# Optimization experiments

Hardware: AMD Instinct MI355X
Metric: run time of the kernel (lower is better)

The kernel has to match this reference:

```python
import jax, jax.numpy as jnp
import numpy as np
from jax import lax


def setup_inputs() -> dict:
    key = jax.random.key(0)
    ks = jax.random.split(key, 16)
    f32 = jnp.float32
    g = lambda k, shp, s=0.02: jax.random.normal(k, shp, dtype=f32) * s
    inp = {
        "x": jax.random.normal(ks[0], (4, 1, 4096), dtype=f32),
        # conv_time: Conv1d(1,128,3,pad=1)
        "conv_time_w": g(ks[1], (128, 1, 3)), "conv_time_b": jnp.zeros((128,), f32),
        "bn0_g": jnp.ones((128,), f32), "bn0_b": jnp.zeros((128,), f32),
        "bn0_m": jnp.zeros((128,), f32), "bn0_v": jnp.ones((128,), f32),
        # block1: Conv1d(128,256,3,pad=1)+BN
        "conv1_w": g(ks[2], (256, 128, 3)), "conv1_b": jnp.zeros((256,), f32),
        "bn1_g": jnp.ones((256,), f32), "bn1_b": jnp.zeros((256,), f32),
        "bn1_m": jnp.zeros((256,), f32), "bn1_v": jnp.ones((256,), f32),
        # block2: Conv1d(256,512,3,pad=1)+BN
        "conv2_w": g(ks[3], (512, 256, 3)), "conv2_b": jnp.zeros((512,), f32),
        "bn2_g": jnp.ones((512,), f32), "bn2_b": jnp.zeros((512,), f32),
        "bn2_m": jnp.zeros((512,), f32), "bn2_v": jnp.ones((512,), f32),
        # GAT 1: fc Linear(512,512), attn_fc Linear(1024,1)
        "gat1_fc_w": g(ks[4], (512, 512)), "gat1_fc_b": jnp.zeros((512,), f32),
        "gat1_attn_w": g(ks[5], (1024,)), "gat1_attn_b": jnp.zeros((), f32),
        # GAT 2: fc Linear(512,256), attn_fc Linear(512,1)
        "gat2_fc_w": g(ks[6], (256, 512)), "gat2_fc_b": jnp.zeros((256,), f32),
        "gat2_attn_w": g(ks[7], (512,)), "gat2_attn_b": jnp.zeros((), f32),
        # head: Linear(256,2)
        "fc_w": g(ks[8], (2, 256)), "fc_b": jnp.zeros((2,), f32),
    }
    return inp


def _conv1d(x, w, b):
    # x: [B,C,T], w: [O,C,3], padding=1
    y = lax.conv_general_dilated(x, w, window_strides=(1,), padding=((1, 1),),
                                 dimension_numbers=("NCH", "OIH", "NCH"))
    return y + b[None, :, None]


def _bn(x, g, b, m, v):
    # eval-mode BatchNorm1d over channel dim
    return (x - m[None, :, None]) * (g * lax.rsqrt(v + 1e-5))[None, :, None] + b[None, :, None]


def _maxpool2(x):
    return lax.reduce_window(x, -jnp.inf, lax.max, (1, 1, 2), (1, 1, 2), "VALID")


def _gat(x2d, fc_w, fc_b, aw, ab):
    # Faithful to: cat([h_i, h_j]) @ attn_w == h_i @ aw[:d] + h_j @ aw[d:]
    h = x2d @ fc_w.T + fc_b           # [N, d]
    d = h.shape[-1]
    s1 = h @ aw[:d]                   # [N] (query part, h.repeat(1,N))
    s2 = h @ aw[d:]                   # [N] (key part,   h.repeat(N,1))
    e = jax.nn.leaky_relu(s1[:, None] + s2[None, :] + ab, negative_slope=0.01)  # [N,N]
    att = jax.nn.softmax(e, axis=1)
    return att @ h                    # [N, d]


def reference(x, conv_time_w, conv_time_b, bn0_g, bn0_b, bn0_m, bn0_v,
              conv1_w, conv1_b, bn1_g, bn1_b, bn1_m, bn1_v,
              conv2_w, conv2_b, bn2_g, bn2_b, bn2_m, bn2_v,
              gat1_fc_w, gat1_fc_b, gat1_attn_w, gat1_attn_b,
              gat2_fc_w, gat2_fc_b, gat2_attn_w, gat2_attn_b,
              fc_w, fc_b):
    h = jax.nn.relu(_bn(_conv1d(x, conv_time_w, conv_time_b), bn0_g, bn0_b, bn0_m, bn0_v))
    h = _maxpool2(jax.nn.relu(_bn(_conv1d(h, conv1_w, conv1_b), bn1_g, bn1_b, bn1_m, bn1_v)))
    h = _maxpool2(jax.nn.relu(_bn(_conv1d(h, conv2_w, conv2_b), bn2_g, bn2_b, bn2_m, bn2_v)))
    h = jnp.transpose(h, (0, 2, 1))   # [B, S, 512]
    B, S, C = h.shape
    g = h.reshape(B * S, C)           # whole batch flattened into one graph (as in source)
    g = _gat(g, gat1_fc_w, gat1_fc_b, gat1_attn_w, gat1_attn_b)   # [N, 512]
    g = _gat(g, gat2_fc_w, gat2_fc_b, gat2_attn_w, gat2_attn_b)   # [N, 256]
    pooled = g.reshape(B, S, -1).mean(axis=1)                     # [B, 256]
    return pooled @ fc_w.T + fc_b     # [B, 2] (dropout is identity in eval)
```

## Files before the change

### kernel.cpp

```cpp
#include <hip/hip_runtime.h>
#include <hip/hip_bf16.h>
#include <math.h>


#define NN 4096
#define BB 4

__global__ void k_conv_time3(const float* __restrict__ x, const float* __restrict__ w,
                             const float* __restrict__ cb, const float* __restrict__ g,
                             const float* __restrict__ bbp, const float* __restrict__ m,
                             const float* __restrict__ v, float* __restrict__ out) {
  int gid = blockIdx.x * 256 + threadIdx.x;
  int t4 = gid & 1023;
  int o = (gid >> 10) & 127;
  int b = gid >> 17;
  int t = t4 * 4;
  float sc = g[o] * rsqrtf(v[o] + 1e-5f);
  float sh = (cb[o] - m[o]) * sc + bbp[o];
  const float* xb = x + b * 4096;
  float4 xc = *(const float4*)&xb[t];
  float xm = (t > 0) ? xb[t - 1] : 0.f;
  float xp = (t + 4 < 4096) ? xb[t + 4] : 0.f;
  const float* wo = w + o * 3;
  float w0 = wo[0], w1 = wo[1], w2 = wo[2];
  float4 y;
  y.x = fmaxf((w0 * xm   + w1 * xc.x + w2 * xc.y) * sc + sh, 0.f);
  y.y = fmaxf((w0 * xc.x + w1 * xc.y + w2 * xc.z) * sc + sh, 0.f);
  y.z = fmaxf((w0 * xc.y + w1 * xc.z + w2 * xc.w) * sc + sh, 0.f);
  y.w = fmaxf((w0 * xc.z + w1 * xc.w + w2 * xp  ) * sc + sh, 0.f);
  float* orow = out + ((size_t)(b * 128) + o) * 4104 + 4;
  *(float4*)&orow[t] = y;
  if (t4 == 0)    { orow[-4] = 0.f; orow[-3] = 0.f; orow[-2] = 0.f; orow[-1] = 0.f; }
  if (t4 == 1023) { orow[4096] = 0.f; orow[4097] = 0.f; orow[4098] = 0.f; orow[4099] = 0.f; }
}

template <int C, int TIN, int OPAD>
__global__ __launch_bounds__(256, 8)
void k_conv_quad(const float* __restrict__ in, const float* __restrict__ w,
                 const float* __restrict__ cb, const float* __restrict__ g,
                 const float* __restrict__ bbp, const float* __restrict__ m,
                 const float* __restrict__ v, float* __restrict__ out, int OCH) {
  constexpr int TOUT = TIN / 2;
  constexpr int IST = TIN + 8;
  constexpr int QC = C / 4;
  const int OST = TOUT + 2 * OPAD;
  __shared__ float red[3][16][64];

  int nT = TIN / 256;
  int bx = blockIdx.x;
  int tb = bx % nT;
  int oq = (bx / nT) % (OCH / 4);
  int b  = bx / (nT * (OCH / 4));
  int tid = threadIdx.x;
  int lane = tid & 63;
  int wv = __builtin_amdgcn_readfirstlane(tid >> 6);
  int t0 = tb * 256;

  float acc[4][4];
  #pragma unroll
  for (int oi = 0; oi < 4; oi++)
    #pragma unroll
    for (int p = 0; p < 4; p++) acc[oi][p] = 0.f;

  const float* wq = w + (size_t)(oq * 4) * C * 3 + (size_t)(wv * QC) * 3;
  const float* xb = in + ((size_t)(b * C) + wv * QC) * IST + 4 + t0 + 4 * lane;

  float4 A = *(const float4*)(xb - 1);
  float2 Bv = *(const float2*)(xb + 3);
  for (int cc = 0; cc < QC; ++cc) {
    float4 An; float2 Bn;
    if (cc + 1 < QC) {
      const float* nx = xb + (size_t)(cc + 1) * IST;
      An = *(const float4*)(nx - 1);
      Bn = *(const float2*)(nx + 3);
    }
    const float* wr = wq + (size_t)cc * 3;
    #pragma unroll
    for (int oi = 0; oi < 4; oi++) {
      const float* wo = wr + (size_t)oi * C * 3;
      float w0 = wo[0], w1 = wo[1], w2 = wo[2];
      acc[oi][0] += w0 * A.x + w1 * A.y + w2 * A.z;
      acc[oi][1] += w0 * A.y + w1 * A.z + w2 * A.w;
      acc[oi][2] += w0 * A.z + w1 * A.w + w2 * Bv.x;
      acc[oi][3] += w0 * A.w + w1 * Bv.x + w2 * Bv.y;
    }
    A = An; Bv = Bn;
  }

  if (wv != 0) {
    #pragma unroll
    for (int oi = 0; oi < 4; oi++)
      #pragma unroll
      for (int p = 0; p < 4; p++)
        red[wv - 1][oi * 4 + p][lane] = acc[oi][p];
  }
  __syncthreads();
  if (wv == 0) {
    int base_o = oq * 4;
    #pragma unroll
    for (int oi = 0; oi < 4; oi++) {
      int o = base_o + oi;
      float sc = g[o] * rsqrtf(v[o] + 1e-5f);
      float sh = (cb[o] - m[o]) * sc + bbp[o];
      float y0 = acc[oi][0] + red[0][oi * 4 + 0][lane] + red[1][oi * 4 + 0][lane] + red[2][oi * 4 + 0][lane];
      float y1 = acc[oi][1] + red[0][oi * 4 + 1][lane] + red[1][oi * 4 + 1][lane] + red[2][oi * 4 + 1][lane];
      float y2 = acc[oi][2] + red[0][oi * 4 + 2][lane] + red[1][oi * 4 + 2][lane] + red[2][oi * 4 + 2][lane];
      float y3 = acc[oi][3] + red[0][oi * 4 + 3][lane] + red[1][oi * 4 + 3][lane] + red[2][oi * 4 + 3][lane];
      float2 r;
      r.x = fmaxf(fmaxf(y0 * sc + sh, y1 * sc + sh), 0.f);
      r.y = fmaxf(fmaxf(y2 * sc + sh, y3 * sc + sh), 0.f);
      *(float2*)&out[((size_t)(b * OCH) + o) * OST + OPAD + tb * 128 + 2 * lane] = r;
    }
    if (OPAD > 0 && tb == 0) {
      if (lane < 4) {
        float* row = out + ((size_t)(b * OCH) + base_o + lane) * OST;
        row[0] = 0.f; row[1] = 0.f; row[2] = 0.f; row[3] = 0.f;
      } else if (lane < 8) {
        float* row = out + ((size_t)(b * OCH) + base_o + lane - 4) * OST;
        row[OPAD + TOUT + 0] = 0.f; row[OPAD + TOUT + 1] = 0.f;
        row[OPAD + TOUT + 2] = 0.f; row[OPAD + TOUT + 3] = 0.f;
      }
    }
  }
}

__global__ __launch_bounds__(512, 4)
void k_gemm_chw(const float* __restrict__ A, const float* __restrict__ Wt,
                const float* __restrict__ bias, float* __restrict__ Cout) {
  constexpr int K = 512, N = 512;
  __shared__ float As[32][132];
  __shared__ float Bs[32][68];
  int i0 = blockIdx.x * 128, j0 = blockIdx.y * 64;
  int tid = threadIdx.x;
  int tx = tid & 15, ty = tid >> 4;
  int b = i0 >> 10, s0 = i0 & 1023;
  const float* Ab = A + (size_t)b * K * 1024 + s0;

  float acc[4][4];
  #pragma unroll
  for (int ii = 0; ii < 4; ii++)
    #pragma unroll
    for (int jj = 0; jj < 4; jj++) acc[ii][jj] = 0.f;

  int ka = (tid + 0) >> 5, i4a = tid & 31;
  int kb = (tid + 512) >> 5, i4b = tid & 31;
  float4 pa0, pa1; float pb[4];

  pa0 = *(const float4*)&Ab[(size_t)ka * 1024 + 4 * i4a];
  pa1 = *(const float4*)&Ab[(size_t)kb * 1024 + 4 * i4b];
  #pragma unroll
  for (int r = 0; r < 4; r++) {
    int e = tid + 512 * r; int j = e >> 5, k = e & 31;
    pb[r] = Wt[(size_t)(j0 + j) * K + k];
  }

  for (int kt = 0; kt < K; kt += 32) {
    *(float4*)&As[ka][4 * i4a] = pa0;
    *(float4*)&As[kb][4 * i4b] = pa1;
    #pragma unroll
    for (int r = 0; r < 4; r++) {
      int e = tid + 512 * r; int j = e >> 5, k = e & 31;
      Bs[k][j] = pb[r];
    }
    __syncthreads();
    int ktn = (kt + 32 < K) ? kt + 32 : 0;
    float4 na0 = *(const float4*)&Ab[(size_t)(ktn + ka) * 1024 + 4 * i4a];
    float4 na1 = *(const float4*)&Ab[(size_t)(ktn + kb) * 1024 + 4 * i4b];
    float nb[4];
    #pragma unroll
    for (int r = 0; r < 4; r++) {
      int e = tid + 512 * r; int j = e >> 5, k = e & 31;
      nb[r] = Wt[(size_t)(j0 + j) * K + ktn + k];
    }
    #pragma unroll 4
    for (int kk = 0; kk < 32; ++kk) {
      float4 a4 = *(const float4*)&As[kk][ty * 4];
      float4 b4 = *(const float4*)&Bs[kk][tx * 4];
      float a[4] = {a4.x, a4.y, a4.z, a4.w};
      float bv[4] = {b4.x, b4.y, b4.z, b4.w};
      #pragma unroll
      for (int ii = 0; ii < 4; ii++)
        #pragma unroll
        for (int jj = 0; jj < 4; jj++) acc[ii][jj] += a[ii] * bv[jj];
    }
    __syncthreads();
    pa0 = na0; pa1 = na1;
    #pragma unroll
    for (int r = 0; r < 4; r++) pb[r] = nb[r];
  }

  float4 bias4 = *(const float4*)&bias[j0 + 4 * tx];
  #pragma unroll
  for (int ii = 0; ii < 4; ii++) {
    int i = i0 + ty * 4 + ii;
    float4 o4;
    o4.x = acc[ii][0] + bias4.x; o4.y = acc[ii][1] + bias4.y;
    o4.z = acc[ii][2] + bias4.z; o4.w = acc[ii][3] + bias4.w;
    *(float4*)&Cout[(size_t)i * N + j0 + 4 * tx] = o4;
  }
}

__global__ __launch_bounds__(256, 4)
void k_gemm_rm(const float* __restrict__ A, const float* __restrict__ Wt,
               const float* __restrict__ bias, float* __restrict__ Cout) {
  constexpr int K = 512, N = 256;
  __shared__ float As[32][68];
  __shared__ float Bs[32][68];
  int i0 = blockIdx.x * 64, j0 = blockIdx.y * 64;
  int tid = threadIdx.x;
  int tx = tid & 15, ty = tid >> 4;

  float acc[4][4];
  #pragma unroll
  for (int ii = 0; ii < 4; ii++)
    #pragma unroll
    for (int jj = 0; jj < 4; jj++) acc[ii][jj] = 0.f;

  float4 pa[2]; float pb[8];
  #pragma unroll
  for (int r = 0; r < 2; r++) {
    int e4 = tid + 256 * r; int i = e4 >> 3, k4 = e4 & 7;
    pa[r] = *(const float4*)&A[(size_t)(i0 + i) * K + 4 * k4];
  }
  #pragma unroll
  for (int r = 0; r < 8; r++) {
    int e = tid + 256 * r; int j = e >> 5, k = e & 31;
    pb[r] = Wt[(size_t)(j0 + j) * K + k];
  }

  for (int kt = 0; kt < K; kt += 32) {
    #pragma unroll
    for (int r = 0; r < 2; r++) {
      int e4 = tid + 256 * r; int i = e4 >> 3, k4 = e4 & 7;
      As[4 * k4 + 0][i] = pa[r].x; As[4 * k4 + 1][i] = pa[r].y;
      As[4 * k4 + 2][i] = pa[r].z; As[4 * k4 + 3][i] = pa[r].w;
    }
    #pragma unroll
    for (int r = 0; r < 8; r++) {
      int e = tid + 256 * r; int j = e >> 5, k = e & 31;
      Bs[k][j] = pb[r];
    }
    __syncthreads();
    int ktn = (kt + 32 < K) ? kt + 32 : 0;
    float4 na[2]; float nb[8];
    #pragma unroll
    for (int r = 0; r < 2; r++) {
      int e4 = tid + 256 * r; int i = e4 >> 3, k4 = e4 & 7;
      na[r] = *(const float4*)&A[(size_t)(i0 + i) * K + ktn + 4 * k4];
    }
    #pragma unroll
    for (int r = 0; r < 8; r++) {
      int e = tid + 256 * r; int j = e >> 5, k = e & 31;
      nb[r] = Wt[(size_t)(j0 + j) * K + ktn + k];
    }
    #pragma unroll 4
    for (int kk = 0; kk < 32; ++kk) {
      float4 a4 = *(const float4*)&As[kk][ty * 4];
      float4 b4 = *(const float4*)&Bs[kk][tx * 4];
      float a[4] = {a4.x, a4.y, a4.z, a4.w};
      float bv[4] = {b4.x, b4.y, b4.z, b4.w};
      #pragma unroll
      for (int ii = 0; ii < 4; ii++)
        #pragma unroll
        for (int jj = 0; jj < 4; jj++) acc[ii][jj] += a[ii] * bv[jj];
    }
    __syncthreads();
    pa[0] = na[0]; pa[1] = na[1];
    #pragma unroll
    for (int r = 0; r < 8; r++) pb[r] = nb[r];
  }

  float4 bias4 = *(const float4*)&bias[j0 + 4 * tx];
  #pragma unroll
  for (int ii = 0; ii < 4; ii++) {
    int i = i0 + ty * 4 + ii;
    float4 o4;
    o4.x = acc[ii][0] + bias4.x; o4.y = acc[ii][1] + bias4.y;
    o4.z = acc[ii][2] + bias4.z; o4.w = acc[ii][3] + bias4.w;
    *(float4*)&Cout[(size_t)i * N + j0 + 4 * tx] = o4;
  }
}

template <int D>
__global__ void k_rowdot(const float* __restrict__ h, const float* __restrict__ aw,
                         float* __restrict__ s1, float* __restrict__ s2,
                         int* __restrict__ rnk) {
  if (blockIdx.x < 16) rnk[blockIdx.x * 256 + threadIdx.x] = 0;
  int wid = threadIdx.x >> 6, lane = threadIdx.x & 63;
  int i = blockIdx.x * 4 + wid;
  const float* hr = h + (size_t)i * D;
  float d1 = 0.f, d2 = 0.f;
  #pragma unroll
  for (int d = lane; d < D; d += 64) {
    float hv = hr[d];
    d1 += hv * aw[d];
    d2 += hv * aw[D + d];
  }
  for (int off = 32; off; off >>= 1) {
    d1 += __shfl_down(d1, off, 64);
    d2 += __shfl_down(d2, off, 64);
  }
  if (lane == 0) { s1[i] = d1; s2[i] = d2; }
}

__global__ void k_rank(const float* __restrict__ s2v, int* __restrict__ rnk) {
  __shared__ float ls[1024];
  int j = blockIdx.x * 256 + threadIdx.x;
  int base = blockIdx.y * 1024;
  float vj = s2v[j];
  for (int e = threadIdx.x; e < 1024; e += 256) ls[e] = s2v[base + e];
  __syncthreads();
  int cnt = 0;
  #pragma unroll 8
  for (int r = 0; r < 1024; ++r) {
    float vr = ls[r];
    cnt += (vr < vj || (vr == vj && (base + r) < j)) ? 1 : 0;
  }
  atomicAdd(&rnk[j], cnt);
}

__global__ void k_scatter(const float* __restrict__ s2v, const int* __restrict__ rnk,
                          float* __restrict__ svals, int* __restrict__ sidx) {
  int j = blockIdx.x * 256 + threadIdx.x;
  int r = rnk[j];
  svals[r] = s2v[j];
  sidx[r] = j;
}

__global__ void k_scan_den(const float* __restrict__ svals,
                           float* __restrict__ preden, float* __restrict__ sufden) {
  __shared__ float csP[256], csM[256];
  int tid = threadIdx.x;
  int base = tid * 16;
  float M2 = svals[NN - 1];
  float lwp[16], lwm[16];
  #pragma unroll
  for (int u = 0; u < 16; u++) {
    float d = svals[base + u] - M2;
    lwp[u] = expf(d);
    lwm[u] = expf(0.01f * d);
  }
  float sm = 0.f, sp = 0.f;
  #pragma unroll
  for (int u = 0; u < 16; u++) { sm += lwm[u]; sp += lwp[u]; }
  csM[tid] = sm; csP[tid] = sp;
  __syncthreads();
  float offM = 0.f;
  for (int c = 0; c < tid; c++) offM += csM[c];
  float offP = 0.f;
  for (int c = tid + 1; c < 256; c++) offP += csP[c];
  float run = offM;
  #pragma unroll
  for (int u = 0; u < 16; u++) { preden[base + u] = run; run += lwm[u]; }
  if (tid == 255) preden[NN] = run;
  float runp = offP;
  if (tid == 255) sufden[NN] = 0.f;
  #pragma unroll
  for (int u = 15; u >= 0; u--) { runp += lwp[u]; sufden[base + u] = runp; }
}

template <int D>
__global__ void k_chunksum(const float* __restrict__ h, const int* __restrict__ sidx,
                           const float* __restrict__ svals,
                           float* __restrict__ csP, float* __restrict__ csM) {
  constexpr int CPT = D / 256;
  int c = blockIdx.x, tid = threadIdx.x;
  __shared__ int lidx[32];
  __shared__ float lwp[32], lwm[32];
  if (tid < 32) {
    int r = c * 32 + tid;
    float d = svals[r] - svals[NN - 1];
    lidx[tid] = sidx[r]; lwp[tid] = expf(d); lwm[tid] = expf(0.01f * d);
  }
  __syncthreads();
  float aP[CPT], aM[CPT];
  #pragma unroll
  for (int q = 0; q < CPT; q++) { aP[q] = 0.f; aM[q] = 0.f; }
  for (int u = 0; u < 32; u++) {
    const float* hr = h + (size_t)lidx[u] * D;
    float fp = lwp[u], fm = lwm[u];
    #pragma unroll
    for (int q = 0; q < CPT; q++) {
      float hv = hr[tid + q * 256];
      aP[q] += fp * hv; aM[q] += fm * hv;
    }
  }
  #pragma unroll
  for (int q = 0; q < CPT; q++) {
    csP[(size_t)c * D + tid + q * 256] = aP[q];
    csM[(size_t)c * D + tid + q * 256] = aM[q];
  }
}

template <int D>
__global__ void k_chunkoff(const float* __restrict__ csP, const float* __restrict__ csM,
                           float* __restrict__ offP, float* __restrict__ offM) {
  int d = blockIdx.x * 128 + threadIdx.x;
  float rm = 0.f;
  for (int cb = 0; cb < 128; cb += 16) {
    float vals[16];
    #pragma unroll
    for (int u = 0; u < 16; u++) vals[u] = csM[(size_t)(cb + u) * D + d];
    #pragma unroll
    for (int u = 0; u < 16; u++) { offM[(size_t)(cb + u) * D + d] = rm; rm += vals[u]; }
  }
  float rp = 0.f;
  for (int cb = 127; cb >= 15; cb -= 16) {
    float vals[16];
    #pragma unroll
    for (int u = 0; u < 16; u++) vals[u] = csP[(size_t)(cb - u) * D + d];
    #pragma unroll
    for (int u = 0; u < 16; u++) { offP[(size_t)(cb - u) * D + d] = rp; rp += vals[u]; }
  }
}

template <int D>
__global__ void k_scanwrite(const float* __restrict__ h, const int* __restrict__ sidx,
                            const float* __restrict__ svals,
                            const float* __restrict__ offP, const float* __restrict__ offM,
                            float* __restrict__ Pre, float* __restrict__ Suf) {
  constexpr int CPT = D / 256;
  int c = blockIdx.x, tid = threadIdx.x;
  __shared__ int lidx[32];
  __shared__ float lwp[32], lwm[32];
  if (tid < 32) {
    int r = c * 32 + tid;
    float d = svals[r] - svals[NN - 1];
    lidx[tid] = sidx[r]; lwp[tid] = expf(d); lwm[tid] = expf(0.01f * d);
  }
  __syncthreads();
  float runM[CPT], runP[CPT];
  #pragma unroll
  for (int q = 0; q < CPT; q++) {
    int d = tid + q * 256;
    runM[q] = offM[(size_t)c * D + d];
    runP[q] = offP[(size_t)c * D + d];
  }
  for (int u = 0; u < 32; u++) {
    const float* hr = h + (size_t)lidx[u] * D;
    float fm = lwm[u];
    #pragma unroll
    for (int q = 0; q < CPT; q++) {
      int d = tid + q * 256;
      Pre[(size_t)(c * 32 + u) * D + d] = runM[q];
      runM[q] += fm * hr[d];
    }
  }
  if (c == 127) {
    #pragma unroll
    for (int q = 0; q < CPT; q++) Pre[(size_t)NN * D + tid + q * 256] = runM[q];
    #pragma unroll
    for (int q = 0; q < CPT; q++) Suf[(size_t)NN * D + tid + q * 256] = 0.f;
  }
  for (int u = 31; u >= 0; u--) {
    const float* hr = h + (size_t)lidx[u] * D;
    float fp = lwp[u];
    #pragma unroll
    for (int q = 0; q < CPT; q++) {
      int d = tid + q * 256;
      runP[q] += fp * hr[d];
      Suf[(size_t)(c * 32 + u) * D + d] = runP[q];
    }
  }
}

template <int D>
__global__ void k_apply(const float* __restrict__ Pre, const float* __restrict__ Suf,
                        const float* __restrict__ preden, const float* __restrict__ sufden,
                        const float* __restrict__ s1, const float* __restrict__ svals,
                        const float* __restrict__ abp, float* __restrict__ outg) {
  int i = blockIdx.x;
  float ab = abp[0], M2 = svals[NN - 1];
  float alpha = s1[i] + ab;
  float cthr = -alpha;
  int lo = 0, hi = NN;
  while (lo < hi) {
    int mid = (lo + hi) >> 1;
    if (svals[mid] < cthr) lo = mid + 1; else hi = mid;
  }
  int t = lo;
  float e1 = alpha + M2;
  float gam = fmaxf(e1, 0.01f * e1);
  float A = expf(e1 - gam);
  float Bv = expf(0.01f * e1 - gam);
  float den = A * sufden[t] + Bv * preden[t];
  float inv = 1.f / den;
  const float* Pr = Pre + (size_t)t * D;
  const float* Sr = Suf + (size_t)t * D;
  for (int d = threadIdx.x; d < D; d += 256)
    outg[(size_t)i * D + d] = (A * Sr[d] + Bv * Pr[d]) * inv;
}

__global__ void k_pool(const float* __restrict__ g2, float* __restrict__ pp) {
  int b = blockIdx.x >> 4, ch = blockIdx.x & 15;
  const float* base = g2 + ((size_t)(b * 1024) + ch * 64) * 256 + threadIdx.x;
  float s = 0.f;
  for (int r = 0; r < 64; r++) s += base[(size_t)r * 256];
  pp[(size_t)blockIdx.x * 256 + threadIdx.x] = s;
}

__global__ void k_head2(const float* __restrict__ pp, const float* __restrict__ fcw,
                        const float* __restrict__ fcb, float* __restrict__ out) {
  __shared__ float pooled[4][256];
  int tid = threadIdx.x;
  for (int b = 0; b < 4; b++) {
    float s = 0.f;
    for (int ch = 0; ch < 16; ch++) s += pp[(size_t)(b * 16 + ch) * 256 + tid];
    pooled[b][tid] = s * (1.f / 1024.f);
  }
  __syncthreads();
  if (tid < 8) {
    int b = tid >> 1, c = tid & 1;
    float acc = fcb[c];
    for (int cc = 0; cc < 256; cc++) acc += pooled[b][cc] * fcw[c * 256 + cc];
    out[b * 2 + c] = acc;
  }
}

extern "C" void kernel_launch(void* const* d_in, const int* in_sizes, int n_in,
                              void* d_out, int out_size, void* d_ws, size_t ws_size,
                              hipStream_t stream) {
  const float* x    = (const float*)d_in[0];
  const float* ctw  = (const float*)d_in[1];
  const float* ctb  = (const float*)d_in[2];
  const float* bn0g = (const float*)d_in[3];
  const float* bn0b = (const float*)d_in[4];
  const float* bn0m = (const float*)d_in[5];
  const float* bn0v = (const float*)d_in[6];
  const float* c1w  = (const float*)d_in[7];
  const float* c1b  = (const float*)d_in[8];
  const float* bn1g = (const float*)d_in[9];
  const float* bn1b = (const float*)d_in[10];
  const float* bn1m = (const float*)d_in[11];
  const float* bn1v = (const float*)d_in[12];
  const float* c2w  = (const float*)d_in[13];
  const float* c2b  = (const float*)d_in[14];
  const float* bn2g = (const float*)d_in[15];
  const float* bn2b = (const float*)d_in[16];
  const float* bn2m = (const float*)d_in[17];
  const float* bn2v = (const float*)d_in[18];
  const float* g1w  = (const float*)d_in[19];
  const float* g1b  = (const float*)d_in[20];
  const float* g1aw = (const float*)d_in[21];
  const float* g1ab = (const float*)d_in[22];
  const float* g2w  = (const float*)d_in[23];
  const float* g2b  = (const float*)d_in[24];
  const float* g2aw = (const float*)d_in[25];
  const float* g2ab = (const float*)d_in[26];
  const float* fcw  = (const float*)d_in[27];
  const float* fcb  = (const float*)d_in[28];
  float* ws = (float*)d_ws;

  const size_t S0SZ = (size_t)4 * 128 * 4104;
  const size_t S1SZ = (size_t)4 * 256 * 2056;
  const size_t SLOT = (size_t)(NN + 1) * 512;
  float* slot0 = ws;
  float* slot1 = ws + S0SZ;
  float* slot2 = slot1 + S1SZ;
  float* slot3 = slot2 + SLOT;
  float* sm    = slot3 + SLOT;
  float* s1    = sm;
  float* s2    = sm + 4096;
  float* svals = sm + 8192;
  int*   sidx  = (int*)(sm + 12288);
  float* preden = sm + 16384;
  float* sufden = sm + 20488;
  float* csP   = sm + 24592;
  float* csM   = csP + 65536;
  float* offP  = csM + 65536;
  float* offM  = offP + 65536;
  int*   rnk   = (int*)(offM + 65536);
  float* pp    = offM + 65536 + 4096;

  k_conv_time3<<<BB * 128 * 1024 / 256, 256, 0, stream>>>(x, ctw, ctb, bn0g, bn0b, bn0m, bn0v, slot0);
  k_conv_quad<128, 4096, 4><<<BB * 64 * 16, 256, 0, stream>>>(
      slot0, c1w, c1b, bn1g, bn1b, bn1m, bn1v, slot1, 256);
  k_conv_quad<256, 2048, 0><<<BB * 128 * 8, 256, 0, stream>>>(
      slot1, c2w, c2b, bn2g, bn2b, bn2m, bn2v, slot2, 512);

  k_gemm_chw<<<dim3(32, 8), 512, 0, stream>>>(slot2, g1w, g1b, slot3);
  k_rowdot<512><<<NN / 4, 256, 0, stream>>>(slot3, g1aw, s1, s2, rnk);
  k_rank<<<dim3(16, 4), 256, 0, stream>>>(s2, rnk);
  k_scatter<<<16, 256, 0, stream>>>(s2, rnk, svals, sidx);
  k_scan_den<<<1, 256, 0, stream>>>(svals, preden, sufden);
  k_chunksum<512><<<128, 256, 0, stream>>>(slot3, sidx, svals, csP, csM);
  k_chunkoff<512><<<4, 128, 0, stream>>>(csP, csM, offP, offM);
  k_scanwrite<512><<<128, 256, 0, stream>>>(slot3, sidx, svals, offP, offM, slot1, slot0);
  k_apply<512><<<NN, 256, 0, stream>>>(slot1, slot0, preden, sufden, s1, svals, g1ab, slot2);

  k_gemm_rm<<<dim3(64, 4), 256, 0, stream>>>(slot2, g2w, g2b, slot3);
  k_rowdot<256><<<NN / 4, 256, 0, stream>>>(slot3, g2aw, s1, s2, rnk);
  k_rank<<<dim3(16, 4), 256, 0, stream>>>(s2, rnk);
  k_scatter<<<16, 256, 0, stream>>>(s2, rnk, svals, sidx);
  k_scan_den<<<1, 256, 0, stream>>>(svals, preden, sufden);
  k_chunksum<256><<<128, 256, 0, stream>>>(slot3, sidx, svals, csP, csM);
  k_chunkoff<256><<<2, 128, 0, stream>>>(csP, csM, offP, offM);
  k_scanwrite<256><<<128, 256, 0, stream>>>(slot3, sidx, svals, offP, offM, slot1, slot0);
  k_apply<256><<<NN, 256, 0, stream>>>(slot1, slot0, preden, sufden, s1, svals, g2ab, slot2);

  k_pool<<<BB * 16, 256, 0, stream>>>(slot2, pp);
  k_head2<<<1, 256, 0, stream>>>(pp, fcw, fcb, (float*)d_out);
}
```

Before: 379.6 us.

## Recast conv1/conv2 as shared-memory tiled implicit GEMM with reordered weights

Replaces the direct per-channel convolution kernel, which splits channels across waves and reduces partial sums through LDS, with an implicit-GEMM formulation. Weights are reordered to [O][tap][C] so K = 3*C runs contiguously, and 64x64 output tiles are built from 32-deep K slabs staged in shared memory with register prefetch of the next slab. The goal is to reuse each loaded input and weight across many outputs and raise arithmetic intensity. The cost is two extra weight-reorder launches per call, more sync points, and lower occupancy from the launch bound dropping to 4.

```diff
diff --git a/kernel.cpp b/kernel.cpp
--- a/kernel.cpp
+++ b/kernel.cpp
@@ -34,92 +34,118 @@
   if (t4 == 1023) { orow[4096] = 0.f; orow[4097] = 0.f; orow[4098] = 0.f; orow[4099] = 0.f; }
 }
 
+template <int C>
+__global__ void k_wreorder(const float* __restrict__ w, float* __restrict__ wr, int OCH) {
+  int idx = blockIdx.x * 256 + threadIdx.x;
+  int K = 3 * C;
+  int o = idx / K;
+  int r = idx - o * K;
+  int k = r / C;
+  int c = r - k * C;
+  wr[idx] = w[((size_t)o * C + c) * 3 + k];
+}
+
 template <int C, int TIN, int OPAD>
-__global__ __launch_bounds__(256, 8)
-void k_conv_quad(const float* __restrict__ in, const float* __restrict__ w,
+__global__ __launch_bounds__(256, 4)
+void k_conv_gemm(const float* __restrict__ xin, const float* __restrict__ wr,
                  const float* __restrict__ cb, const float* __restrict__ g,
                  const float* __restrict__ bbp, const float* __restrict__ m,
                  const float* __restrict__ v, float* __restrict__ out, int OCH) {
+  constexpr int K = 3 * C;
   constexpr int TOUT = TIN / 2;
   constexpr int IST = TIN + 8;
-  constexpr int QC = C / 4;
   const int OST = TOUT + 2 * OPAD;
-  __shared__ float red[3][16][64];
-
-  int nT = TIN / 256;
+  __shared__ float As[32][68];
+  __shared__ float Bs[32][68];
+
+  int nT = TIN / 64;
   int bx = blockIdx.x;
   int tb = bx % nT;
-  int oq = (bx / nT) % (OCH / 4);
-  int b  = bx / (nT * (OCH / 4));
+  int oq = (bx / nT) % (OCH / 64);
+  int b  = bx / (nT * (OCH / 64));
+  int o0 = oq * 64;
+  int t0 = tb * 64;
   int tid = threadIdx.x;
-  int lane = tid & 63;
-  int wv = __builtin_amdgcn_readfirstlane(tid >> 6);
-  int t0 = tb * 256;
+  int tx = tid & 15, ty = tid >> 4;
+
+  const float* xbase = xin + (size_t)(b * C) * IST + 4 + t0;
 
   float acc[4][4];
   #pragma unroll
-  for (int oi = 0; oi < 4; oi++)
-    #pragma unroll
-    for (int p = 0; p < 4; p++) acc[oi][p] = 0.f;
-
-  const float* wq = w + (size_t)(oq * 4) * C * 3 + (size_t)(wv * QC) * 3;
-  const float* xb = in + ((size_t)(b * C) + wv * QC) * IST + 4 + t0 + 4 * lane;
-
-  float4 A = *(const float4*)(xb - 1);
-  float2 Bv = *(const float2*)(xb + 3);
-  for (int cc = 0; cc < QC; ++cc) {
-    float4 An; float2 Bn;
-    if (cc + 1 < QC) {
-      const float* nx = xb + (size_t)(cc + 1) * IST;
-      An = *(const float4*)(nx - 1);
-      Bn = *(const float2*)(nx + 3);
-    }
-    const float* wr = wq + (size_t)cc * 3;
-    #pragma unroll
-    for (int oi = 0; oi < 4; oi++) {
-      const float* wo = wr + (size_t)oi * C * 3;
-      float w0 = wo[0], w1 = wo[1], w2 = wo[2];
-      acc[oi][0] += w0 * A.x + w1 * A.y + w2 * A.z;
-      acc[oi][1] += w0 * A.y + w1 * A.z + w2 * A.w;
-      acc[oi][2] += w0 * A.z + w1 * A.w + w2 * Bv.x;
-      acc[oi][3] += w0 * A.w + w1 * Bv.x + w2 * Bv.y;
-    }
-    A = An; Bv = Bn;
-  }
-
-  if (wv != 0) {
-    #pragma unroll
-    for (int oi = 0; oi < 4; oi++)
+  for (int ii = 0; ii < 4; ii++)
+    #pragma unroll
+    for (int jj = 0; jj < 4; jj++) acc[ii][jj] = 0.f;
+
+  float4 pa[2], pb[2];
+  #pragma unroll
+  for (int r = 0; r < 2; r++) {
+    int e4 = tid + 256 * r;
+    int i = e4 >> 3, k4 = e4 & 7;
+    pa[r] = *(const float4*)&wr[(size_t)(o0 + i) * K + 4 * k4];
+    int kk = e4 >> 4, j4 = e4 & 15;
+    pb[r] = *(const float4*)&xbase[(size_t)kk * IST + 4 * j4 - 1];
+  }
+
+  for (int kt = 0; kt < K; kt += 32) {
+    #pragma unroll
+    for (int r = 0; r < 2; r++) {
+      int e4 = tid + 256 * r;
+      int i = e4 >> 3, k4 = e4 & 7;
+      As[4 * k4 + 0][i] = pa[r].x; As[4 * k4 + 1][i] = pa[r].y;
+      As[4 * k4 + 2][i] = pa[r].z; As[4 * k4 + 3][i] = pa[r].w;
+      int kk = e4 >> 4, j4 = e4 & 15;
+      *(float4*)&Bs[kk][4 * j4] = pb[r];
+    }
+    __syncthreads();
+    int ktn = (kt + 32 < K) ? kt + 32 : 0;
+    int ktap = ktn / C, c0 = ktn - ktap * C;
+    float4 na[2], nb[2];
+    #pragma unroll
+    for (int r = 0; r < 2; r++) {
+      int e4 = tid + 256 * r;
+      int i = e4 >> 3, k4 = e4 & 7;
+      na[r] = *(const float4*)&wr[(size_t)(o0 + i) * K + ktn + 4 * k4];
+      int kk = e4 >> 4, j4 = e4 & 15;
+      nb[r] = *(const float4*)&xbase[(size_t)(c0 + kk) * IST + 4 * j4 + ktap - 1];
+    }
+    #pragma unroll 4
+    for (int kk = 0; kk < 32; ++kk) {
+      float4 a4 = *(const float4*)&As[kk][ty * 4];
+      float4 b4 = *(const float4*)&Bs[kk][tx * 4];
+      float a[4] = {a4.x, a4.y, a4.z, a4.w};
+      float bv[4] = {b4.x, b4.y, b4.z, b4.w};
       #pragma unroll
-      for (int p = 0; p < 4; p++)
-        red[wv - 1][oi * 4 + p][lane] = acc[oi][p];
-  }
-  __syncthreads();
-  if (wv == 0) {
-    int base_o = oq * 4;
-    #pragma unroll
-    for (int oi = 0; oi < 4; oi++) {
-      int o = base_o + oi;
-      float sc = g[o] * rsqrtf(v[o] + 1e-5f);
-      float sh = (cb[o] - m[o]) * sc + bbp[o];
-      float y0 = acc[oi][0] + red[0][oi * 4 + 0][lane] + red[1][oi * 4 + 0][lane] + red[2][oi * 4 + 0][lane];
-      float y1 = acc[oi][1] + red[0][oi * 4 + 1][lane] + red[1][oi * 4 + 1][lane] + red[2][oi * 4 + 1][lane];
-      float y2 = acc[oi][2] + red[0][oi * 4 + 2][lane] + red[1][oi * 4 + 2][lane] + red[2][oi * 4 + 2][lane];
-      float y3 = acc[oi][3] + red[0][oi * 4 + 3][lane] + red[1][oi * 4 + 3][lane] + red[2][oi * 4 + 3][lane];
-      float2 r;
-      r.x = fmaxf(fmaxf(y0 * sc + sh, y1 * sc + sh), 0.f);
-      r.y = fmaxf(fmaxf(y2 * sc + sh, y3 * sc + sh), 0.f);
-      *(float2*)&out[((size_t)(b * OCH) + o) * OST + OPAD + tb * 128 + 2 * lane] = r;
-    }
-    if (OPAD > 0 && tb == 0) {
-      if (lane < 4) {
-        float* row = out + ((size_t)(b * OCH) + base_o + lane) * OST;
-        row[0] = 0.f; row[1] = 0.f; row[2] = 0.f; row[3] = 0.f;
-      } else if (lane < 8) {
-        float* row = out + ((size_t)(b * OCH) + base_o + lane - 4) * OST;
-        row[OPAD + TOUT + 0] = 0.f; row[OPAD + TOUT + 1] = 0.f;
-        row[OPAD + TOUT + 2] = 0.f; row[OPAD + TOUT + 3] = 0.f;
-      }
+      for (int ii = 0; ii < 4; ii++)
+        #pragma unroll
+        for (int jj = 0; jj < 4; jj++) acc[ii][jj] += a[ii] * bv[jj];
+    }
+    __syncthreads();
+    pa[0] = na[0]; pa[1] = na[1];
+    pb[0] = nb[0]; pb[1] = nb[1];
+  }
+
+  #pragma unroll
+  for (int ii = 0; ii < 4; ii++) {
+    int o = o0 + ty * 4 + ii;
+    float sc = g[o] * rsqrtf(v[o] + 1e-5f);
+    float sh = (cb[o] - m[o]) * sc + bbp[o];
+    float y0 = acc[ii][0] * sc + sh;
+    float y1 = acc[ii][1] * sc + sh;
+    float y2 = acc[ii][2] * sc + sh;
+    float y3 = acc[ii][3] * sc + sh;
+    float2 r;
+    r.x = fmaxf(fmaxf(y0, y1), 0.f);
+    r.y = fmaxf(fmaxf(y2, y3), 0.f);
+    *(float2*)&out[((size_t)(b * OCH) + o) * OST + OPAD + t0 / 2 + tx * 2] = r;
+  }
+  if (OPAD > 0 && tb == 0) {
+    if (tid < 64) {
+      float* row = out + ((size_t)(b * OCH) + o0 + tid) * OST;
+      row[0] = 0.f; row[1] = 0.f; row[2] = 0.f; row[3] = 0.f;
+    } else if (tid < 128) {
+      float* row = out + ((size_t)(b * OCH) + o0 + tid - 64) * OST;
+      row[OPAD + TOUT + 0] = 0.f; row[OPAD + TOUT + 1] = 0.f;
+      row[OPAD + TOUT + 2] = 0.f; row[OPAD + TOUT + 3] = 0.f;
     }
   }
 }
@@ -571,12 +597,17 @@
   float* offM  = offP + 65536;
   int*   rnk   = (int*)(offM + 65536);
   float* pp    = offM + 65536 + 4096;
+  float* wr1   = pp + 16384;
+  float* wr2   = wr1 + 98304;
+
+  k_wreorder<128><<<(256 * 384) / 256, 256, 0, stream>>>(c1w, wr1, 256);
+  k_wreorder<256><<<(512 * 768) / 256, 256, 0, stream>>>(c2w, wr2, 512);
 
   k_conv_time3<<<BB * 128 * 1024 / 256, 256, 0, stream>>>(x, ctw, ctb, bn0g, bn0b, bn0m, bn0v, slot0);
-  k_conv_quad<128, 4096, 4><<<BB * 64 * 16, 256, 0, stream>>>(
-      slot0, c1w, c1b, bn1g, bn1b, bn1m, bn1v, slot1, 256);
-  k_conv_quad<256, 2048, 0><<<BB * 128 * 8, 256, 0, stream>>>(
-      slot1, c2w, c2b, bn2g, bn2b, bn2m, bn2v, slot2, 512);
+  k_conv_gemm<128, 4096, 4><<<BB * 4 * 64, 256, 0, stream>>>(
+      slot0, wr1, c1b, bn1g, bn1b, bn1m, bn1v, slot1, 256);
+  k_conv_gemm<256, 2048, 0><<<BB * 8 * 32, 256, 0, stream>>>(
+      slot1, wr2, c2b, bn2g, bn2b, bn2m, bn2v, slot2, 512);
 
   k_gemm_chw<<<dim3(32, 8), 512, 0, stream>>>(slot2, g1w, g1b, slot3);
   k_rowdot<512><<<NN / 4, 256, 0, stream>>>(slot3, g1aw, s1, s2, rnk);
```

Result: slower. 418.6 us (+10.3%).
